# Kernel optimization log

Measured on AMD Instinct MI355X. Metric: run time of the kernel, lower is better.

## Reference

```python
import jax, jax.numpy as jnp
import numpy as np

M, N, D, L, DEPTH, WIDTH, BATCH = 64, 4096, 64, 32, 4, 256, 1024
WIN = 2 * L + 1


def setup_inputs() -> dict:
    key = jax.random.key(0)
    ks = jax.random.split(key, 5)
    u = jax.random.normal(ks[0], (BATCH, D), dtype=jnp.float32)
    # xavier-style scaled gaussians for weights, zeros for biases (matches torch init pattern)
    weight0 = jax.random.normal(ks[1], (M, WIDTH, D), dtype=jnp.float32) * (2.0 / (WIDTH + D)) ** 0.5
    bias0 = jnp.zeros((M, WIDTH, 1), dtype=jnp.float32)
    weight = jax.random.normal(ks[2], (DEPTH - 1, M, WIDTH, WIDTH), dtype=jnp.float32) * (1.0 / WIDTH) ** 0.5
    bias = jnp.zeros((DEPTH - 1, M, WIDTH, 1), dtype=jnp.float32)
    weight_final = jax.random.normal(ks[3], (M, WIN, WIDTH), dtype=jnp.float32) * (2.0 / (WIN + WIDTH)) ** 0.5
    bias_final = jnp.zeros((M, WIN, 1), dtype=jnp.float32)
    xi = jax.random.normal(ks[4], (M, N + 2 * L), dtype=jnp.float32) * (2.0 / (M + N + 2 * L)) ** 0.5
    return {"u": u, "weight0": weight0, "bias0": bias0, "weight": weight,
            "bias": bias, "weight_final": weight_final, "bias_final": bias_final, "xi": xi}


def reference(u, weight0, bias0, weight, bias, weight_final, bias_final, xi) -> jnp.ndarray:
    act = jax.nn.sigmoid
    # per-M shared MLP: u1 [M, width, batch]
    u1 = act(jnp.einsum('mwd,bd->mwb', weight0, u) + bias0)
    for i in range(weight.shape[0]):  # small fixed depth loop
        u1 = act(jnp.einsum('mwv,mvb->mwb', weight[i], u1) + bias[i])
    G = act(jnp.einsum('mjw,mwb->mjb', weight_final, u1) + bias_final)
    # sliding-window correlation: out[n, b] = sum_{m,j} xi[m, n+j] * G[m, j, b]
    win = G.shape[1]
    n_out = xi.shape[1] - (win - 1)
    idx = jnp.arange(n_out)[:, None] + jnp.arange(win)[None, :]
    xw = xi[:, idx]
    return jnp.einsum('mnj,mjb->nb', xw, G)  # [N, batch]
```

## Files before the change

kernel.cpp:

```cpp
#include <hip/hip_runtime.h>
#include <math.h>

typedef __attribute__((ext_vector_type(8))) short short8;
typedef __attribute__((ext_vector_type(4))) float floatx4;

__device__ __forceinline__ void load_lds16(const void* g, void* l) {
    __builtin_amdgcn_global_load_lds((const __attribute__((address_space(1))) void*)g,
                                     (__attribute__((address_space(3))) void*)l,
                                     16, 0, 0);
}

__device__ __forceinline__ unsigned short f2bf(float x) {
    union { float f; unsigned int u; } v; v.f = x;
    unsigned int r = v.u + 0x7fffu + ((v.u >> 16) & 1u);
    return (unsigned short)(r >> 16);
}

__device__ __forceinline__ unsigned int pack_bf(float f0, float f1) {
    union { float f; unsigned int u; } a, b;
    a.f = f0; b.f = f1;
    return __builtin_amdgcn_perm(b.u + 0x8000u, a.u + 0x8000u, 0x07060302u);
}

__device__ __forceinline__ float fast_exp2(float x) {
#if __has_builtin(__builtin_amdgcn_exp2f)
    return __builtin_amdgcn_exp2f(x);
#else
    return __expf(x * 0.69314718056f);
#endif
}

__device__ __forceinline__ float fast_rcp(float x) {
#if __has_builtin(__builtin_amdgcn_rcpf)
    return __builtin_amdgcn_rcpf(x);
#else
    return 1.0f / x;
#endif
}

#define NEG_LOG2E (-1.4426950408889634f)

__global__ void prep(const float* __restrict__ w0, const float* __restrict__ w,
                     const float* __restrict__ wf, const float* __restrict__ xi,
                     unsigned short* __restrict__ w0d, unsigned short* __restrict__ wd,
                     unsigned short* __restrict__ wfd, unsigned int* __restrict__ xw) {
    const int bid = blockIdx.x;
    if (bid < 6656) {
        const bool is0 = bid < 512;
        const int c = (is0 ? bid : bid - 512) * 256 + threadIdx.x;
        const int cpm = is0 ? 2048 : 8192;
        const int Kk  = is0 ? 2 : 8;
        const int K   = Kk * 32;
        const int mm  = c / cpm;
        const int cm  = c - mm * cpm;
        const int rblk = cm / (Kk * 64);
        const int rem  = cm - rblk * (Kk * 64);
        const int kk   = rem >> 6;
        const int lane = rem & 63;
        const int r  = rblk * 16 + (lane & 15);
        const int k0 = kk * 32 + (lane >> 4) * 8;
        const float* srcp = (is0 ? w0 : w) + ((size_t)mm * 256 + r) * K + k0;
        unsigned short* dstp = (is0 ? w0d : wd) + (size_t)c * 8;
        float4 a = *(const float4*)srcp;
        float4 b = *(const float4*)(srcp + 4);
        short8 o = { (short)f2bf(a.x), (short)f2bf(a.y), (short)f2bf(a.z), (short)f2bf(a.w),
                     (short)f2bf(b.x), (short)f2bf(b.y), (short)f2bf(b.z), (short)f2bf(b.w) };
        *(short8*)dstp = o;
    } else if (bid < 7680) {
        const int c = (bid - 6656) * 256 + threadIdx.x;
        const int m  = c >> 12;
        const int cm = c & 4095;
        const int rblk = cm >> 9;
        const int rem  = cm & 511;
        const int kk   = rem >> 6;
        const int lane = rem & 63;
        const int r  = rblk * 16 + (lane & 15);
        const int k0 = kk * 32 + (lane >> 4) * 8;
        short8 o = {0,0,0,0,0,0,0,0};
        if (r < 65) {
            const float* srcp = wf + ((size_t)m * 65 + r) * 256 + k0;
            float4 a = *(const float4*)srcp;
            float4 b = *(const float4*)(srcp + 4);
            o = (short8){ (short)f2bf(a.x), (short)f2bf(a.y), (short)f2bf(a.z), (short)f2bf(a.w),
                          (short)f2bf(b.x), (short)f2bf(b.y), (short)f2bf(b.z), (short)f2bf(b.w) };
        }
        *(short8*)(wfd + (size_t)c * 8) = o;
    } else {
        const int n = bid - 7680;
        #pragma unroll
        for (int t = 0; t < 9; ++t) {
            const int idx = t * 256 + threadIdx.x;
            if (idx < 2176) {
                const int m = idx / 34;
                const int pos = idx - m * 34;
                const int j0 = pos * 2;
                const float* xim = xi + (size_t)m * 4160 + n;
                const float v0 = (j0 < 65) ? xim[j0] : 0.0f;
                const float v1 = (j0 + 1 < 65) ? xim[j0 + 1] : 0.0f;
                xw[(size_t)n * 2176 + idx] =
                    (unsigned int)f2bf(v0) | ((unsigned int)f2bf(v1) << 16);
            }
        }
    }
}

template<int K, int I>
__device__ __forceinline__ void load_w(
    const unsigned short* __restrict__ Wt, int wave, int lane, short8 (&w)[I][K / 32])
{
    constexpr int Kk = K / 32;
    const unsigned short* wb = Wt + ((size_t)(wave * I * Kk) * 64 + lane) * 8;
    #pragma unroll
    for (int i = 0; i < I; ++i)
        #pragma unroll
        for (int kk = 0; kk < Kk; ++kk)
            w[i][kk] = *(const short8*)(wb + (size_t)(i * Kk + kk) * 512);
}

template<int K, int I>
__device__ __forceinline__ void mfma_tile(
    const short8 (&w)[I][K / 32], const unsigned short* src, int t,
    int quad, int l16, floatx4 (&acc)[I][4])
{
    constexpr int Kk = K / 32;
    #pragma unroll
    for (int i = 0; i < I; ++i)
        #pragma unroll
        for (int j = 0; j < 4; ++j) acc[i][j] = (floatx4){0.f, 0.f, 0.f, 0.f};
    #pragma unroll
    for (int kk = 0; kk < Kk; ++kk) {
        short8 bf[4];
        #pragma unroll
        for (int j = 0; j < 4; ++j) {
            const int cb = t * 64 + j * 16 + l16;
            bf[j] = *(const short8*)&src[cb * K + (((kk * 4 + quad) ^ (cb & 7)) * 8)];
        }
        #pragma unroll
        for (int i = 0; i < I; ++i)
            #pragma unroll
            for (int j = 0; j < 4; ++j)
                acc[i][j] = __builtin_amdgcn_mfma_f32_16x16x32_bf16(w[i][kk], bf[j], acc[i][j], 0, 0, 0);
    }
}

template<int I>
__device__ __forceinline__ void mlp_write_t(
    const float* __restrict__ bm, unsigned short* dst, int t,
    int wave, int quad, int l16, floatx4 (&acc)[I][4])
{
    const int rbw = wave * (I * 16);
    #pragma unroll
    for (int i = 0; i < I; ++i) {
        const int rb = rbw + i * 16 + quad * 4;
        float c0 = bm[rb]     * NEG_LOG2E;
        float c1 = bm[rb + 1] * NEG_LOG2E;
        float c2 = bm[rb + 2] * NEG_LOG2E;
        float c3 = bm[rb + 3] * NEG_LOG2E;
        #pragma unroll
        for (int j = 0; j < 4; ++j) {
            const int cb = t * 64 + j * 16 + l16;
            float r0 = fast_rcp(1.0f + fast_exp2(fmaf(acc[i][j][0], NEG_LOG2E, c0)));
            float r1 = fast_rcp(1.0f + fast_exp2(fmaf(acc[i][j][1], NEG_LOG2E, c1)));
            float r2 = fast_rcp(1.0f + fast_exp2(fmaf(acc[i][j][2], NEG_LOG2E, c2)));
            float r3 = fast_rcp(1.0f + fast_exp2(fmaf(acc[i][j][3], NEG_LOG2E, c3)));
            uint2 o = { pack_bf(r0, r1), pack_bf(r2, r3) };
            *(uint2*)&dst[cb * 256 + (((rb >> 3) ^ (cb & 7)) * 8) + (rb & 7)] = o;
        }
    }
}

__global__ __launch_bounds__(256, 2)
void fused_mlp(const float* __restrict__ u,
               const unsigned short* __restrict__ w0_bf, const float* __restrict__ b0_,
               const unsigned short* __restrict__ w_bf,  const float* __restrict__ b_,
               const unsigned short* __restrict__ wf_bf, const float* __restrict__ bf_,
               unsigned short* __restrict__ Gflat) {
    __shared__ unsigned short X[128 * 256];

    const int bid = blockIdx.x;
    const int xcd = bid & 7, slot = bid >> 3;
    const int m  = (xcd << 3) + (slot >> 3);
    const int b0 = (slot & 7) << 7;
    const int tid = threadIdx.x, wave = tid >> 6, lane = tid & 63;
    const int quad = lane >> 4, l16 = lane & 15;

    {
        const int b = tid >> 1, hk = tid & 1;
        const float* up = u + (size_t)(b0 + b) * 64 + hk * 32;
        #pragma unroll
        for (int c = 0; c < 4; ++c) {
            float4 v0 = *(const float4*)(up + c * 8);
            float4 v1 = *(const float4*)(up + c * 8 + 4);
            uint4 p = { pack_bf(v0.x, v0.y), pack_bf(v0.z, v0.w),
                        pack_bf(v1.x, v1.y), pack_bf(v1.z, v1.w) };
            *(uint4*)&X[b * 64 + (((hk * 4 + c) ^ (b & 7)) * 8)] = p;
        }
    }
    __syncthreads();

    floatx4 acc[4][4];

    {
        short8 w0r[4][2];
        load_w<64, 4>(w0_bf + (size_t)m * 16384, wave, lane, w0r);
        floatx4 acc2[4][4];
        mfma_tile<64, 4>(w0r, X, 0, quad, l16, acc);
        mfma_tile<64, 4>(w0r, X, 1, quad, l16, acc2);
        __syncthreads();
        mlp_write_t<4>(b0_ + (size_t)m * 256, X, 0, wave, quad, l16, acc);
        mlp_write_t<4>(b0_ + (size_t)m * 256, X, 1, wave, quad, l16, acc2);
        __syncthreads();
    }

    #pragma unroll 1
    for (int l = 0; l < 3; ++l) {
        short8 wr[4][8];
        load_w<256, 4>(w_bf + ((size_t)l * 64 + m) * 65536, wave, lane, wr);
        const float* bm = b_ + ((size_t)l * 64 + m) * 256;
        mfma_tile<256, 4>(wr, X, 0, quad, l16, acc);
        __syncthreads();
        mlp_write_t<4>(bm, X, 0, wave, quad, l16, acc);
        mfma_tile<256, 4>(wr, X, 1, quad, l16, acc);
        __syncthreads();
        mlp_write_t<4>(bm, X, 1, wave, quad, l16, acc);
    }
    __syncthreads();

    {
        short8 wfr[2][8];
        load_w<256, 2>(wf_bf + (size_t)m * 32768, wave, lane, wfr);
        const float* bm = bf_ + (size_t)m * 65;
        unsigned short* Gg = Gflat + (size_t)b0 * 4352 + m * 68;
        floatx4 acf[2][4];
        #pragma unroll
        for (int t = 0; t < 2; ++t) {
            mfma_tile<256, 2>(wfr, X, t, quad, l16, acf);
            #pragma unroll
            for (int i = 0; i < 2; ++i) {
                const int rb = wave * 32 + i * 16 + quad * 4;
                if (rb < 68) {
                    float c[4];
                    #pragma unroll
                    for (int rr = 0; rr < 4; ++rr)
                        c[rr] = (rb + rr < 65) ? bm[rb + rr] * NEG_LOG2E : 0.0f;
                    #pragma unroll
                    for (int j = 0; j < 4; ++j) {
                        const int cb = t * 64 + j * 16 + l16;
                        float r0 = fast_rcp(1.0f + fast_exp2(fmaf(acf[i][j][0], NEG_LOG2E, c[0])));
                        float r1 = fast_rcp(1.0f + fast_exp2(fmaf(acf[i][j][1], NEG_LOG2E, c[1])));
                        float r2 = fast_rcp(1.0f + fast_exp2(fmaf(acf[i][j][2], NEG_LOG2E, c[2])));
                        float r3 = fast_rcp(1.0f + fast_exp2(fmaf(acf[i][j][3], NEG_LOG2E, c[3])));
                        uint2 o = { pack_bf(r0, r1), pack_bf(r2, r3) };
                        *(uint2*)&Gg[(size_t)cb * 4352 + rb] = o;
                    }
                }
            }
        }
    }
}

__global__ __launch_bounds__(256, 2)
void contract_gemm(const unsigned short* __restrict__ XW,
                   const unsigned short* __restrict__ G,
                   float* __restrict__ out) {
    const int bid = blockIdx.x;
    const int xcd = bid & 7, slot = bid >> 3;
    const int r0 = ((xcd << 2) + (slot >> 4)) << 7;
    const int c0 = (slot & 15) << 6;

    __shared__ unsigned short As[128 * 64];
    __shared__ unsigned short Bs[64 * 64];

    const int tid = threadIdx.x;
    const int wave = tid >> 6, lane = tid & 63;
    const int quad = lane >> 4, l16 = lane & 15;
    const int wr = (wave & 1) * 64;
    const int wc = (wave >> 1) * 32;
    const int lrow = lane >> 3;
    const int spos = lane & 7;

    floatx4 acc[4][2];
    #pragma unroll
    for (int i = 0; i < 4; ++i)
        #pragma unroll
        for (int j = 0; j < 2; ++j) acc[i][j] = (floatx4){0.f, 0.f, 0.f, 0.f};

    for (int k0 = 0; k0 < 4352; k0 += 64) {
        #pragma unroll
        for (int t = 0; t < 4; ++t) {
            const int row = wave * 32 + t * 8 + lrow;
            const int fc  = spos ^ (row & 7);
            load_lds16(XW + (size_t)(r0 + row) * 4352 + k0 + fc * 8,
                       &As[(wave * 32 + t * 8) * 64]);
        }
        #pragma unroll
        for (int t = 0; t < 2; ++t) {
            const int row = wave * 16 + t * 8 + lrow;
            const int fc  = spos ^ (row & 7);
            load_lds16(G + (size_t)(c0 + row) * 4352 + k0 + fc * 8,
                       &Bs[(wave * 16 + t * 8) * 64]);
        }
        __syncthreads();

        #pragma unroll
        for (int kk = 0; kk < 2; ++kk) {
            short8 af[4], bfr[2];
            #pragma unroll
            for (int i = 0; i < 4; ++i) {
                const int ra = wr + i * 16 + l16;
                af[i]  = *(const short8*)&As[ra * 64 + (((kk * 4 + quad) ^ (ra & 7)) * 8)];
            }
            #pragma unroll
            for (int j = 0; j < 2; ++j) {
                const int cb = wc + j * 16 + l16;
                bfr[j] = *(const short8*)&Bs[cb * 64 + (((kk * 4 + quad) ^ (cb & 7)) * 8)];
            }
            #pragma unroll
            for (int i = 0; i < 4; ++i)
                #pragma unroll
                for (int j = 0; j < 2; ++j)
                    acc[i][j] = __builtin_amdgcn_mfma_f32_16x16x32_bf16(af[i], bfr[j], acc[i][j], 0, 0, 0);
        }
        __syncthreads();
    }

    #pragma unroll
    for (int i = 0; i < 4; ++i) {
        const int rb = r0 + wr + i * 16 + quad * 4;
        #pragma unroll
        for (int rr = 0; rr < 4; ++rr)
            #pragma unroll
            for (int j = 0; j < 2; ++j) {
                const int col = c0 + wc + j * 16 + l16;
                out[(size_t)(rb + rr) * 1024 + col] = acc[i][j][rr];
            }
    }
}

extern "C" void kernel_launch(void* const* d_in, const int* in_sizes, int n_in,
                              void* d_out, int out_size, void* d_ws, size_t ws_size,
                              hipStream_t stream) {
    const float* u   = (const float*)d_in[0];
    const float* w0  = (const float*)d_in[1];
    const float* b0_ = (const float*)d_in[2];
    const float* w   = (const float*)d_in[3];
    const float* b   = (const float*)d_in[4];
    const float* wf  = (const float*)d_in[5];
    const float* bf_ = (const float*)d_in[6];
    const float* xi  = (const float*)d_in[7];
    float* out = (float*)d_out;

    unsigned short* w0_bf = (unsigned short*)d_ws;
    unsigned short* w_bf  = w0_bf + 1048576;
    unsigned short* wf_bf = w_bf  + 12582912;
    unsigned short* Gflat = wf_bf + 2097152;
    unsigned short* XW    = Gflat + 4456448;

    prep<<<11776, 256, 0, stream>>>(w0, w, wf, xi, w0_bf, w_bf, wf_bf, (unsigned int*)XW);
    fused_mlp<<<512, 256, 0, stream>>>(u, w0_bf, b0_, w_bf, b, wf_bf, bf_, Gflat);
    contract_gemm<<<512, 256, 0, stream>>>(XW, Gflat, out);
}
```

Before: 218.9 us.

## Pre-swizzle XW into MFMA fragment layout and double-buffer contraction GEMM

The prep kernel now writes the sliding-window xi matrix straight into MFMA A-fragment order, so the contraction GEMM can load A operands from global memory into registers without going through LDS. The contraction tile grows to 128x128 per block with 4x4 accumulators per wave, and B tiles are double-buffered in LDS so the next tile loads while the current one computes. The grid halves to 256 blocks and prep launches fewer xi blocks, each covering 16 output rows. The cost is higher register pressure (launch bounds allow one block per CU) and fewer blocks to spread across the CUs.

Measured after the change: 295.1 us. 1.35x slower.

```diff
diff --git a/kernel.cpp b/kernel.cpp
--- a/kernel.cpp
+++ b/kernel.cpp
@@ -43,7 +43,7 @@
 __global__ void prep(const float* __restrict__ w0, const float* __restrict__ w,
                      const float* __restrict__ wf, const float* __restrict__ xi,
                      unsigned short* __restrict__ w0d, unsigned short* __restrict__ wd,
-                     unsigned short* __restrict__ wfd, unsigned int* __restrict__ xw) {
+                     unsigned short* __restrict__ wfd, unsigned short* __restrict__ xwf) {
     const int bid = blockIdx.x;
     if (bid < 6656) {
         const bool is0 = bid < 512;
@@ -86,20 +86,22 @@
         }
         *(short8*)(wfd + (size_t)c * 8) = o;
     } else {
-        const int n = bid - 7680;
-        #pragma unroll
-        for (int t = 0; t < 9; ++t) {
-            const int idx = t * 256 + threadIdx.x;
-            if (idx < 2176) {
-                const int m = idx / 34;
-                const int pos = idx - m * 34;
-                const int j0 = pos * 2;
-                const float* xim = xi + (size_t)m * 4160 + n;
-                const float v0 = (j0 < 65) ? xim[j0] : 0.0f;
-                const float v1 = (j0 + 1 < 65) ? xim[j0 + 1] : 0.0f;
-                xw[(size_t)n * 2176 + idx] =
-                    (unsigned int)f2bf(v0) | ((unsigned int)f2bf(v1) << 16);
+        const int nblk = bid - 7680;
+        const int lane = threadIdx.x & 63, wv = threadIdx.x >> 6;
+        const int n = (nblk << 4) + (lane & 15);
+        const int koff = (lane >> 4) << 3;
+        unsigned short* dst = xwf + ((size_t)nblk * 136 * 64 + lane) * 8;
+        for (int r = wv; r < 136; r += 4) {
+            const int k0 = r * 32 + koff;
+            short8 o;
+            #pragma unroll
+            for (int e = 0; e < 8; ++e) {
+                const int k = k0 + e;
+                const int m = k / 68;
+                const int j = k - m * 68;
+                o[e] = (j < 65) ? (short)f2bf(xi[(size_t)m * 4160 + n + j]) : (short)0;
             }
+            *(short8*)(dst + (size_t)r * 512) = o;
         }
     }
 }
@@ -259,68 +261,92 @@
     }
 }
 
-__global__ __launch_bounds__(256, 2)
-void contract_gemm(const unsigned short* __restrict__ XW,
+__device__ __forceinline__ void stage_b(
+    const unsigned short* __restrict__ G, unsigned short* Bsb,
+    int c0, int k0, int wave, int lrow, int spos)
+{
+    #pragma unroll
+    for (int t = 0; t < 4; ++t) {
+        const int row = wave * 32 + t * 8 + lrow;
+        const int fc  = spos ^ (row & 7);
+        load_lds16(G + (size_t)(c0 + row) * 4352 + k0 + fc * 8,
+                   Bsb + (wave * 32 + t * 8) * 64);
+    }
+}
+
+__device__ __forceinline__ void load_a(
+    const unsigned short* __restrict__ Abase, int kt, short8 (&af)[8])
+{
+    #pragma unroll
+    for (int i = 0; i < 4; ++i)
+        #pragma unroll
+        for (int kk = 0; kk < 2; ++kk)
+            af[kk * 4 + i] = *(const short8*)(Abase + (size_t)(i * 136 + kt * 2 + kk) * 512);
+}
+
+__device__ __forceinline__ void comp_frag(
+    const short8 (&af)[8], const unsigned short* Bsb,
+    int wc, int quad, int l16, floatx4 (&acc)[4][4])
+{
+    #pragma unroll
+    for (int kk = 0; kk < 2; ++kk) {
+        short8 bfr[4];
+        #pragma unroll
+        for (int j = 0; j < 4; ++j) {
+            const int cb = wc + j * 16 + l16;
+            bfr[j] = *(const short8*)&Bsb[cb * 64 + (((kk * 4 + quad) ^ (cb & 7)) * 8)];
+        }
+        #pragma unroll
+        for (int i = 0; i < 4; ++i)
+            #pragma unroll
+            for (int j = 0; j < 4; ++j)
+                acc[i][j] = __builtin_amdgcn_mfma_f32_16x16x32_bf16(af[kk * 4 + i], bfr[j], acc[i][j], 0, 0, 0);
+    }
+}
+
+__global__ __launch_bounds__(256, 1)
+void contract_gemm(const unsigned short* __restrict__ XWf,
                    const unsigned short* __restrict__ G,
                    float* __restrict__ out) {
     const int bid = blockIdx.x;
     const int xcd = bid & 7, slot = bid >> 3;
-    const int r0 = ((xcd << 2) + (slot >> 4)) << 7;
-    const int c0 = (slot & 15) << 6;
-
-    __shared__ unsigned short As[128 * 64];
-    __shared__ unsigned short Bs[64 * 64];
+    const int r0 = ((xcd << 2) + (slot >> 3)) << 7;
+    const int c0 = (slot & 7) << 7;
+
+    __shared__ unsigned short Bs[2][128 * 64];
 
     const int tid = threadIdx.x;
     const int wave = tid >> 6, lane = tid & 63;
     const int quad = lane >> 4, l16 = lane & 15;
     const int wr = (wave & 1) * 64;
-    const int wc = (wave >> 1) * 32;
-    const int lrow = lane >> 3;
-    const int spos = lane & 7;
-
-    floatx4 acc[4][2];
+    const int wc = (wave >> 1) * 64;
+    const int lrow = lane >> 3, spos = lane & 7;
+
+    const unsigned short* Abase =
+        XWf + ((size_t)(((r0 + wr) >> 4) * 136) * 64 + lane) * 8;
+
+    floatx4 acc[4][4];
     #pragma unroll
     for (int i = 0; i < 4; ++i)
         #pragma unroll
-        for (int j = 0; j < 2; ++j) acc[i][j] = (floatx4){0.f, 0.f, 0.f, 0.f};
-
-    for (int k0 = 0; k0 < 4352; k0 += 64) {
-        #pragma unroll
-        for (int t = 0; t < 4; ++t) {
-            const int row = wave * 32 + t * 8 + lrow;
-            const int fc  = spos ^ (row & 7);
-            load_lds16(XW + (size_t)(r0 + row) * 4352 + k0 + fc * 8,
-                       &As[(wave * 32 + t * 8) * 64]);
-        }
-        #pragma unroll
-        for (int t = 0; t < 2; ++t) {
-            const int row = wave * 16 + t * 8 + lrow;
-            const int fc  = spos ^ (row & 7);
-            load_lds16(G + (size_t)(c0 + row) * 4352 + k0 + fc * 8,
-                       &Bs[(wave * 16 + t * 8) * 64]);
-        }
-        __syncthreads();
-
-        #pragma unroll
-        for (int kk = 0; kk < 2; ++kk) {
-            short8 af[4], bfr[2];
-            #pragma unroll
-            for (int i = 0; i < 4; ++i) {
-                const int ra = wr + i * 16 + l16;
-                af[i]  = *(const short8*)&As[ra * 64 + (((kk * 4 + quad) ^ (ra & 7)) * 8)];
-            }
-            #pragma unroll
-            for (int j = 0; j < 2; ++j) {
-                const int cb = wc + j * 16 + l16;
-                bfr[j] = *(const short8*)&Bs[cb * 64 + (((kk * 4 + quad) ^ (cb & 7)) * 8)];
-            }
-            #pragma unroll
-            for (int i = 0; i < 4; ++i)
-                #pragma unroll
-                for (int j = 0; j < 2; ++j)
-                    acc[i][j] = __builtin_amdgcn_mfma_f32_16x16x32_bf16(af[i], bfr[j], acc[i][j], 0, 0, 0);
-        }
+        for (int j = 0; j < 4; ++j) acc[i][j] = (floatx4){0.f, 0.f, 0.f, 0.f};
+
+    short8 afA[8], afB[8];
+
+    stage_b(G, Bs[0], c0, 0, wave, lrow, spos);
+    load_a(Abase, 0, afA);
+    __syncthreads();
+
+    for (int t = 0; t < 68; t += 2) {
+        stage_b(G, Bs[1], c0, (t + 1) * 64, wave, lrow, spos);
+        load_a(Abase, t + 1, afB);
+        comp_frag(afA, Bs[0], wc, quad, l16, acc);
+        __syncthreads();
+        if (t + 2 < 68) {
+            stage_b(G, Bs[0], c0, (t + 2) * 64, wave, lrow, spos);
+            load_a(Abase, t + 2, afA);
+        }
+        comp_frag(afB, Bs[1], wc, quad, l16, acc);
         __syncthreads();
     }
 
@@ -330,7 +356,7 @@
         #pragma unroll
         for (int rr = 0; rr < 4; ++rr)
             #pragma unroll
-            for (int j = 0; j < 2; ++j) {
+            for (int j = 0; j < 4; ++j) {
                 const int col = c0 + wc + j * 16 + l16;
                 out[(size_t)(rb + rr) * 1024 + col] = acc[i][j][rr];
             }
@@ -354,9 +380,9 @@
     unsigned short* w_bf  = w0_bf + 1048576;
     unsigned short* wf_bf = w_bf  + 12582912;
     unsigned short* Gflat = wf_bf + 2097152;
-    unsigned short* XW    = Gflat + 4456448;
-
-    prep<<<11776, 256, 0, stream>>>(w0, w, wf, xi, w0_bf, w_bf, wf_bf, (unsigned int*)XW);
+    unsigned short* XWf   = Gflat + 4456448;
+
+    prep<<<7936, 256, 0, stream>>>(w0, w, wf, xi, w0_bf, w_bf, wf_bf, XWf);
     fused_mlp<<<512, 256, 0, stream>>>(u, w0_bf, b0_, w_bf, b, wf_bf, bf_, Gflat);
-    contract_gemm<<<512, 256, 0, stream>>>(XW, Gflat, out);
-}
+    contract_gemm<<<256, 256, 0, stream>>>(XWf, Gflat, out);
+}
```
